# Kernel optimization log

Hardware: AMD Instinct MI355X
Metric: run time of the kernel (lower is better)

## Reference

```python
import jax, jax.numpy as jnp
import numpy as np
from jax import lax

T, B, V, E, HID, K = 512, 256, 50000, 300, 512, 9
H = HID // 2  # per-direction LSTM hidden size


def setup_inputs() -> dict:
    key = jax.random.key(0)
    ks = jax.random.split(key, 16)
    input_ids = jax.random.randint(ks[0], (T, B), 0, V, dtype=jnp.int32)
    lens = jax.random.randint(ks[1], (B,), T // 2, T + 1, dtype=jnp.int32)
    seq_lengths = jnp.sort(lens)[::-1].at[0].set(T)  # sorted desc, max == T
    label_ids = jax.random.randint(ks[2], (T, B), 0, K, dtype=jnp.int32)
    s = 0.1
    emb_table = jax.random.normal(ks[3], (V, E), jnp.float32) * s
    W_ih_f = jax.random.normal(ks[4], (4 * H, E), jnp.float32) * s
    W_hh_f = jax.random.normal(ks[5], (4 * H, H), jnp.float32) * s
    b_f = jax.random.normal(ks[6], (4 * H,), jnp.float32) * s  # b_ih + b_hh fused
    W_ih_b = jax.random.normal(ks[7], (4 * H, E), jnp.float32) * s
    W_hh_b = jax.random.normal(ks[8], (4 * H, H), jnp.float32) * s
    b_b = jax.random.normal(ks[9], (4 * H,), jnp.float32) * s
    W_out = jax.random.normal(ks[10], (K, HID), jnp.float32) * s
    b_out = jax.random.normal(ks[11], (K,), jnp.float32) * s
    start_trans = jax.random.normal(ks[12], (K,), jnp.float32) * s
    end_trans = jax.random.normal(ks[13], (K,), jnp.float32) * s
    trans = jax.random.normal(ks[14], (K, K), jnp.float32) * s
    return dict(input_ids=input_ids, seq_lengths=seq_lengths, label_ids=label_ids,
                emb_table=emb_table, W_ih_f=W_ih_f, W_hh_f=W_hh_f, b_f=b_f,
                W_ih_b=W_ih_b, W_hh_b=W_hh_b, b_b=b_b, W_out=W_out, b_out=b_out,
                start_trans=start_trans, end_trans=end_trans, trans=trans)


def _run_lstm(x, maskf, W_ih, W_hh, b, reverse):
    # x: [T,B,E], maskf: [T,B] float. Precompute input projections (one big GEMM).
    xg = jnp.einsum('tbe,ge->tbg', x, W_ih) + b  # [T,B,4H]

    def step(carry, inp):
        h, c = carry
        xg_t, m = inp
        gates = xg_t + h @ W_hh.T
        i, f, g, o = jnp.split(gates, 4, axis=-1)
        c_new = jax.nn.sigmoid(f) * c + jax.nn.sigmoid(i) * jnp.tanh(g)
        h_new = jax.nn.sigmoid(o) * jnp.tanh(c_new)
        m = m[:, None]
        return (m * h_new + (1 - m) * h, m * c_new + (1 - m) * c), m * h_new + (1 - m) * h

    init = (jnp.zeros((B, H), x.dtype), jnp.zeros((B, H), x.dtype))
    _, hs = lax.scan(step, init, (xg, maskf), reverse=reverse)
    return hs  # [T,B,H]


def reference(input_ids, seq_lengths, label_ids, emb_table, W_ih_f, W_hh_f, b_f,
              W_ih_b, W_hh_b, b_b, W_out, b_out, start_trans, end_trans, trans):
    maskf = (jnp.arange(T)[:, None] < seq_lengths[None, :]).astype(emb_table.dtype)  # [T,B]
    maskb = maskf.astype(bool)

    embeds = emb_table[input_ids]  # [T,B,E]
    h_f = _run_lstm(embeds, maskf, W_ih_f, W_hh_f, b_f, reverse=False)
    h_b = _run_lstm(embeds, maskf, W_ih_b, W_hh_b, b_b, reverse=True)
    lstm_out = jnp.concatenate([h_f, h_b], axis=-1)  # [T,B,HID]
    emissions = jnp.einsum('tbh,kh->tbk', lstm_out, W_out) + b_out  # [T,B,K]

    b_idx = jnp.arange(B)
    # --- CRF numerator (gold path score) ---
    num = start_trans[label_ids[0]] + emissions[0, b_idx, label_ids[0]]
    trans_sc = trans[label_ids[:-1], label_ids[1:]]  # [T-1,B]
    emit_sc = jnp.take_along_axis(emissions[1:], label_ids[1:, :, None], axis=2)[..., 0]
    num = num + jnp.sum((trans_sc + emit_sc) * maskf[1:], axis=0)
    last_tags = label_ids[seq_lengths - 1, b_idx]
    num = num + end_trans[last_tags]

    # --- CRF denominator (forward algorithm, log-sum-exp scan) ---
    def fwd_step(alpha, inp):
        em_t, m = inp
        nxt = jax.nn.logsumexp(alpha[:, :, None] + trans[None], axis=1) + em_t
        return jnp.where(m[:, None].astype(bool), nxt, alpha), None

    alpha0 = start_trans[None] + emissions[0]  # [B,K]
    alpha, _ = lax.scan(fwd_step, alpha0, (emissions[1:], maskf[1:]))
    denom = jax.nn.logsumexp(alpha + end_trans[None], axis=1)
    loss = -jnp.sum(num - denom)  # torchcrf reduction='sum', model negates llh

    # --- Viterbi decode ---
    def vit_step(score, inp):
        em_t, m = inp
        brd = score[:, :, None] + trans[None]  # [B,K_prev,K_next]
        idx = jnp.argmax(brd, axis=1)          # [B,K]
        nxt = jnp.max(brd, axis=1) + em_t
        return jnp.where(m[:, None].astype(bool), nxt, score), idx

    score0 = start_trans[None] + emissions[0]
    score, hist = lax.scan(vit_step, score0, (emissions[1:], maskf[1:]))  # hist [T-1,B,K]
    best_last = jnp.argmax(score + end_trans[None], axis=1)  # [B] tag at last valid pos

    def back_step(tag, inp):
        h_t, m_next = inp
        new = jnp.where(m_next.astype(bool),
                        jnp.take_along_axis(h_t, tag[:, None], axis=1)[:, 0],
                        best_last)
        return new, new

    _, preds = lax.scan(back_step, best_last, (hist, maskf[1:]), reverse=True)  # [T-1,B]
    pred_ids = jnp.concatenate([preds, best_last[None]], axis=0)  # [T,B]
    pred_ids = jnp.where(maskb, pred_ids, 0)
    return loss, pred_ids
```

## Files before the change

### kernel.cpp

```cpp
#include <hip/hip_runtime.h>
#include <math.h>

#define TT 512
#define BB 256
#define EE 300
#define KK 9
#define HH 256
#define GG 1024
#define CHS 64
#define NCH (TT/CHS)

#define OFF_XG ((size_t)0)
#define OFF_WT (OFF_XG + (size_t)2*CHS*BB*GG)
#define OFF_HS (OFF_WT + (size_t)2*64*1024*4)
#define OFF_CS (OFF_HS + (size_t)2*BB*HH)
#define OFF_EF (OFF_CS + (size_t)2*BB*HH)
#define OFF_EB (OFF_EF + (size_t)BB*TT*KK)
#define OFF_ND (OFF_EB + (size_t)BB*TT*KK)

#define DOT4(a_,b_) ((a_).x*(b_).x + (a_).y*(b_).y + (a_).z*(b_).z + (a_).w*(b_).w)
#define FMA4(acc_, w_, h_) do { \
    acc_ = fmaf((w_).x, (h_).x, acc_); \
    acc_ = fmaf((w_).y, (h_).y, acc_); \
    acc_ = fmaf((w_).z, (h_).z, acc_); \
    acc_ = fmaf((w_).w, (h_).w, acc_); } while (0)

__global__ __launch_bounds__(1024) void wtrans_kernel(
    const float* __restrict__ Wf, const float* __restrict__ Wb, float* __restrict__ Wt)
{
  int idx = blockIdx.x * 1024 + threadIdx.x;
  int dir = idx >> 16;
  int r   = (idx >> 6) & 1023;
  int k4  = idx & 63;
  const float* W = dir ? Wb : Wf;
  float4 v = *(const float4*)&W[(size_t)r * HH + k4 * 4];
  ((float4*)Wt)[(size_t)dir * 65536 + (size_t)k4 * 1024 + r] = v;
}

__global__ __launch_bounds__(256) void gemm_xg_kernel(
    const int* __restrict__ ids, const float* __restrict__ emb,
    const float* __restrict__ W_ih_f, const float* __restrict__ W_ih_b,
    const float* __restrict__ b_f, const float* __restrict__ b_b,
    float* __restrict__ xgc, int ci)
{
  __shared__ float As[60][132];
  __shared__ float Ws[60][132];
  __shared__ int tokid[128];
  const int tid = threadIdx.x;
  const int bx  = blockIdx.x;
  const int dir = bx >> 8;
  const int rem = bx & 255;
  const int rt  = rem & 127;
  const int nth = rem >> 7;
  const float* W_ih = dir ? W_ih_b : W_ih_f;
  const float* bias = dir ? b_b : b_f;

  if (tid < 128) {
    int m = rt * 128 + tid;
    int sidx = ci * CHS + (m >> 8);
    int t = dir ? (TT - 1 - sidx) : sidx;
    tokid[tid] = ids[t * BB + (m & 255)];
  }
  __syncthreads();

  const int ty = tid >> 4, tx = tid & 15;
  for (int nt = nth * 4; nt < nth * 4 + 4; ++nt) {
    float acc[8][8];
    #pragma unroll
    for (int a_ = 0; a_ < 8; ++a_)
      #pragma unroll
      for (int b_ = 0; b_ < 8; ++b_) acc[a_][b_] = 0.f;

    for (int kc = 0; kc < 5; ++kc) {
      __syncthreads();
      for (int i = tid; i < 128 * 15; i += 256) {
        int mm = i / 15, kq = i - mm * 15;
        float4 v = *(const float4*)&emb[(size_t)tokid[mm] * EE + kc * 60 + kq * 4];
        As[kq*4+0][mm] = v.x; As[kq*4+1][mm] = v.y;
        As[kq*4+2][mm] = v.z; As[kq*4+3][mm] = v.w;
      }
      for (int i = tid; i < 128 * 15; i += 256) {
        int nn = i / 15, kq = i - nn * 15;
        float4 v = *(const float4*)&W_ih[(size_t)(nt*128+nn) * EE + kc * 60 + kq * 4];
        Ws[kq*4+0][nn] = v.x; Ws[kq*4+1][nn] = v.y;
        Ws[kq*4+2][nn] = v.z; Ws[kq*4+3][nn] = v.w;
      }
      __syncthreads();
      for (int kk = 0; kk < 60; ++kk) {
        float4 a0 = *(const float4*)&As[kk][ty*8];
        float4 a1 = *(const float4*)&As[kk][ty*8+4];
        float4 w0 = *(const float4*)&Ws[kk][tx*8];
        float4 w1 = *(const float4*)&Ws[kk][tx*8+4];
        float av[8]  = {a0.x,a0.y,a0.z,a0.w,a1.x,a1.y,a1.z,a1.w};
        float wv8[8] = {w0.x,w0.y,w0.z,w0.w,w1.x,w1.y,w1.z,w1.w};
        #pragma unroll
        for (int im = 0; im < 8; ++im)
          #pragma unroll
          for (int in = 0; in < 8; ++in) acc[im][in] += av[im] * wv8[in];
      }
    }
    #pragma unroll
    for (int im = 0; im < 8; ++im) {
      int m = ty*8 + im;
      int n = nt*128 + tx*8;
      float4 o0, o1;
      o0.x = acc[im][0] + bias[n+0]; o0.y = acc[im][1] + bias[n+1];
      o0.z = acc[im][2] + bias[n+2]; o0.w = acc[im][3] + bias[n+3];
      o1.x = acc[im][4] + bias[n+4]; o1.y = acc[im][5] + bias[n+5];
      o1.z = acc[im][6] + bias[n+6]; o1.w = acc[im][7] + bias[n+7];
      float* dst = &xgc[(size_t)(dir*16384 + rt*128 + m) * GG + n];
      *(float4*)dst = o0; *(float4*)(dst+4) = o1;
    }
  }
}

__global__ __launch_bounds__(1024, 1) void rec_chunk_kernel(
    const float* __restrict__ xgc, const float* __restrict__ Wt,
    const int* __restrict__ lens,
    float* __restrict__ hst, float* __restrict__ cst,
    float* __restrict__ emisf, float* __restrict__ emisb,
    const float* __restrict__ W_out, const float* __restrict__ b_out, int ci)
{
  __shared__ __align__(16) float hring[2][2][272];
  __shared__ __align__(16) float Wo[KK][256];

  const int tid  = threadIdx.x;
  const int bid  = blockIdx.x;
  const int dir  = (bid & 7) >> 2;
  const int grp  = (bid >> 3) * 4 + (bid & 3);
  const int b0   = grp * 2;
  const int lane = tid & 63;
  const int wv   = tid >> 6;
  const int rg   = wv * 16 + (lane & 15);
  const int kseg = (lane >> 4) & 3;
  const bool cellLane = (lane & 48) == 0;
  float* emis = dir ? emisb : emisf;

  for (int i = tid; i < KK * 64; i += 1024) {
    int k = i >> 6, q = i & 63;
    *(float4*)&Wo[k][q*4] = *(const float4*)&W_out[(size_t)k * 512 + dir*256 + q*4];
  }

  int eb = 0, ek = 0, es = 0;
  const bool edo = tid < 2 * KK * 16;
  if (edo) { int q = tid; eb = q / 144; q -= eb * 144; ek = q >> 4; es = q & 15; }
  const float ebias = (edo && dir == 0) ? b_out[ek] : 0.f;

  int len2[2];
  #pragma unroll
  for (int b = 0; b < 2; ++b) len2[b] = lens[b0 + b];

  float creg[2] = {0.f,0.f}, hreg[2] = {0.f,0.f};
  if (cellLane) {
    if (ci > 0) {
      #pragma unroll
      for (int b = 0; b < 2; ++b) {
        hreg[b] = hst[((size_t)dir*BB + b0 + b) * HH + rg];
        creg[b] = cst[((size_t)dir*BB + b0 + b) * HH + rg];
      }
    }
    #pragma unroll
    for (int b = 0; b < 2; ++b)
      hring[0][b][rg + ((rg >> 6) << 2)] = hreg[b];
  }
  __syncthreads();

  const float4* wp = (const float4*)Wt + (size_t)dir * 65536
                   + (size_t)(kseg * 16) * 1024 + rg;

  for (int sl = 0; sl < CHS; ++sl) {
    const int s = ci * CHS + sl;
    const int t = dir ? (TT - 1 - s) : s;
    const int cur = sl & 1, nxt = cur ^ 1;

    float xv[4][2];
    if (cellLane) {
      const float* xb = xgc + ((size_t)dir*(CHS*BB) + (size_t)sl*BB + b0) * GG + rg;
      #pragma unroll
      for (int q = 0; q < 4; ++q)
        #pragma unroll
        for (int b = 0; b < 2; ++b)
          xv[q][b] = __builtin_nontemporal_load(&xb[(size_t)b * GG + q * 256]);
    }

    float acc[4][2];
    #pragma unroll
    for (int q = 0; q < 4; ++q) { acc[q][0] = 0.f; acc[q][1] = 0.f; }

    const float4* hb = (const float4*)&hring[0][0][0] + cur * (2*68) + kseg * 17;
    float4 w0 = wp[0], w1 = wp[256], w2 = wp[512], w3 = wp[768];
    #pragma unroll 5
    for (int i = 0; i < 15; ++i) {
      const float4* wn = wp + (size_t)(i + 1) * 1024;
      float4 n0 = wn[0], n1 = wn[256], n2 = wn[512], n3 = wn[768];
      float4 h0 = hb[i], h1 = hb[68 + i];
      FMA4(acc[0][0], w0, h0); FMA4(acc[0][1], w0, h1);
      FMA4(acc[1][0], w1, h0); FMA4(acc[1][1], w1, h1);
      FMA4(acc[2][0], w2, h0); FMA4(acc[2][1], w2, h1);
      FMA4(acc[3][0], w3, h0); FMA4(acc[3][1], w3, h1);
      w0 = n0; w1 = n1; w2 = n2; w3 = n3;
    }
    {
      float4 h0 = hb[15], h1 = hb[68 + 15];
      FMA4(acc[0][0], w0, h0); FMA4(acc[0][1], w0, h1);
      FMA4(acc[1][0], w1, h0); FMA4(acc[1][1], w1, h1);
      FMA4(acc[2][0], w2, h0); FMA4(acc[2][1], w2, h1);
      FMA4(acc[3][0], w3, h0); FMA4(acc[3][1], w3, h1);
    }

    #pragma unroll
    for (int q = 0; q < 4; ++q)
      #pragma unroll
      for (int b = 0; b < 2; ++b) {
        float v = acc[q][b];
        v += __shfl_xor(v, 16);
        v += __shfl_xor(v, 32);
        acc[q][b] = v;
      }

    if (cellLane) {
      #pragma unroll
      for (int b = 0; b < 2; ++b) {
        float gi = acc[0][b] + xv[0][b];
        float gf = acc[1][b] + xv[1][b];
        float gg = acc[2][b] + xv[2][b];
        float go = acc[3][b] + xv[3][b];
        float si = 1.f / (1.f + expf(-gi));
        float sf = 1.f / (1.f + expf(-gf));
        float so = 1.f / (1.f + expf(-go));
        float cn = sf * creg[b] + si * tanhf(gg);
        float hn = so * tanhf(cn);
        bool m = t < len2[b];
        hreg[b] = m ? hn : hreg[b];
        creg[b] = m ? cn : creg[b];
        hring[nxt][b][rg + ((rg >> 6) << 2)] = hreg[b];
      }
    }
    __syncthreads();

    if (edo) {
      float r = 0.f;
      #pragma unroll
      for (int i4 = 0; i4 < 4; ++i4) {
        float4 h4 = *(const float4*)&hring[nxt][eb][es*4 + i4*68];
        float4 w4 = *(const float4*)&Wo[ek][es*4 + i4*64];
        r += DOT4(h4, w4);
      }
      r += __shfl_xor(r, 8); r += __shfl_xor(r, 4);
      r += __shfl_xor(r, 2); r += __shfl_xor(r, 1);
      if (es == 0)
        __builtin_nontemporal_store(r + ebias,
            &emis[((size_t)(b0 + eb) * TT + t) * KK + ek]);
    }
  }

  if (cellLane) {
    #pragma unroll
    for (int b = 0; b < 2; ++b) {
      hst[((size_t)dir*BB + b0 + b) * HH + rg] = hreg[b];
      cst[((size_t)dir*BB + b0 + b) * HH + rg] = creg[b];
    }
  }
}

__global__ __launch_bounds__(64) void crf_kernel(
    const float* __restrict__ emis_f, const float* __restrict__ emis_b2,
    const int* __restrict__ labels, const int* __restrict__ lens,
    const float* __restrict__ start_trans, const float* __restrict__ end_trans,
    const float* __restrict__ trans,
    float* __restrict__ numden, float* __restrict__ outp)
{
  const int b = blockIdx.x;
  const int lane = threadIdx.x;
  __shared__ __align__(16) float em[TT * KK];
  __shared__ unsigned char hist[TT * KK];
  const float4* ef = (const float4*)(emis_f + (size_t)b * TT * KK);
  const float4* eb = (const float4*)(emis_b2 + (size_t)b * TT * KK);
  for (int i = lane; i < TT*KK/4; i += 64) {
    float4 a = ef[i], c = eb[i];
    float4 o; o.x = a.x+c.x; o.y = a.y+c.y; o.z = a.z+c.z; o.w = a.w+c.w;
    ((float4*)em)[i] = o;
  }
  const int len = lens[b];
  const int k = lane < KK ? lane : KK-1;
  float tc[KK];
  #pragma unroll
  for (int jj = 0; jj < KK; ++jj) tc[jj] = trans[jj*KK + k];
  __syncthreads();

  float nacc = 0.f;
  for (int t = lane; t < TT; t += 64) {
    int lt = labels[t*BB + b];
    if (t == 0) nacc += start_trans[lt] + em[lt];
    else if (t < len) nacc += trans[labels[(t-1)*BB + b]*KK + lt] + em[t*KK + lt];
  }
  if (lane == 0) nacc += end_trans[labels[(size_t)(len-1)*BB + b]];
  #pragma unroll
  for (int off = 32; off; off >>= 1) nacc += __shfl_down(nacc, off);

  float alpha[KK], score[KK];
  #pragma unroll
  for (int jj = 0; jj < KK; ++jj) {
    float v = start_trans[jj] + em[jj];
    alpha[jj] = v; score[jj] = v;
  }
  for (int t = 1; t < TT; ++t) {
    float av[KK]; float mx = -1e30f;
    #pragma unroll
    for (int jj = 0; jj < KK; ++jj) { av[jj] = alpha[jj] + tc[jj]; mx = fmaxf(mx, av[jj]); }
    float ssum = 0.f;
    #pragma unroll
    for (int jj = 0; jj < KK; ++jj) ssum += expf(av[jj] - mx);
    float e_tk = em[t*KK + k];
    float na = mx + logf(ssum) + e_tk;
    float best = -1e30f; int bj = 0;
    #pragma unroll
    for (int jj = 0; jj < KK; ++jj) {
      float sv = score[jj] + tc[jj];
      if (sv > best) { best = sv; bj = jj; }
    }
    float ns = best + e_tk;
    bool msk = t < len;
    na = msk ? na : alpha[k];
    ns = msk ? ns : score[k];
    if (lane < KK) hist[(t-1)*KK + lane] = (unsigned char)bj;
    #pragma unroll
    for (int jj = 0; jj < KK; ++jj) { alpha[jj] = __shfl(na, jj); score[jj] = __shfl(ns, jj); }
  }
  float dm = -1e30f;
  #pragma unroll
  for (int jj = 0; jj < KK; ++jj) dm = fmaxf(dm, alpha[jj] + end_trans[jj]);
  float dsum = 0.f;
  #pragma unroll
  for (int jj = 0; jj < KK; ++jj) dsum += expf(alpha[jj] + end_trans[jj] - dm);
  float denom = dm + logf(dsum);
  int bl_ = 0; float bs = -1e30f;
  #pragma unroll
  for (int jj = 0; jj < KK; ++jj) {
    float v = score[jj] + end_trans[jj];
    if (v > bs) { bs = v; bl_ = jj; }
  }
  if (lane == 0) numden[b] = nacc - denom;
  __syncthreads();
  if (lane == 0) {
    int tag = bl_;
    outp[1 + (size_t)(TT-1)*BB + b] = ((TT-1) < len) ? (float)bl_ : 0.f;
    for (int s = TT-2; s >= 0; --s) {
      tag = ((s+1) < len) ? (int)hist[s*KK + tag] : bl_;
      outp[1 + (size_t)s*BB + b] = (s < len) ? (float)tag : 0.f;
    }
  }
}

__global__ __launch_bounds__(256) void loss_reduce_kernel(
    const float* __restrict__ numden, float* __restrict__ out)
{
  __shared__ float sh[256];
  int tid = threadIdx.x;
  sh[tid] = numden[tid];
  __syncthreads();
  for (int s = 128; s > 0; s >>= 1) {
    if (tid < s) sh[tid] += sh[tid + s];
    __syncthreads();
  }
  if (tid == 0) out[0] = -sh[0];
}

extern "C" void kernel_launch(void* const* d_in, const int* in_sizes, int n_in,
                              void* d_out, int out_size, void* d_ws, size_t ws_size,
                              hipStream_t stream)
{
  const int*   ids    = (const int*)d_in[0];
  const int*   lens   = (const int*)d_in[1];
  const int*   labels = (const int*)d_in[2];
  const float* emb    = (const float*)d_in[3];
  const float* W_ih_f = (const float*)d_in[4];
  const float* W_hh_f = (const float*)d_in[5];
  const float* b_f    = (const float*)d_in[6];
  const float* W_ih_b = (const float*)d_in[7];
  const float* W_hh_b = (const float*)d_in[8];
  const float* b_b    = (const float*)d_in[9];
  const float* W_out  = (const float*)d_in[10];
  const float* b_out  = (const float*)d_in[11];
  const float* s_tr   = (const float*)d_in[12];
  const float* e_tr   = (const float*)d_in[13];
  const float* trans  = (const float*)d_in[14];
  float* out = (float*)d_out;

  float* ws = (float*)d_ws;
  float* xgc    = ws + OFF_XG;
  float* Wt     = ws + OFF_WT;
  float* hst    = ws + OFF_HS;
  float* cst    = ws + OFF_CS;
  float* emis_f = ws + OFF_EF;
  float* emis_b = ws + OFF_EB;
  float* numden = ws + OFF_ND;

  wtrans_kernel<<<128, 1024, 0, stream>>>(W_hh_f, W_hh_b, Wt);

  for (int ci = 0; ci < NCH; ++ci) {
    gemm_xg_kernel<<<512, 256, 0, stream>>>(ids, emb, W_ih_f, W_ih_b, b_f, b_b, xgc, ci);
    rec_chunk_kernel<<<256, 1024, 0, stream>>>(xgc, Wt, lens, hst, cst,
                                               emis_f, emis_b, W_out, b_out, ci);
  }

  crf_kernel<<<BB, 64, 0, stream>>>(emis_f, emis_b, labels, lens, s_tr, e_tr, trans, numden, out);
  loss_reduce_kernel<<<1, 256, 0, stream>>>(numden, out);
}
```

Before: 7.220 ms.

## Keep part of recurrent weights resident in registers and LDS across timesteps

The recurrent step streams the W_hh slice from global memory every timestep. This keeps the first 3 of 16 k-blocks in registers (48 floats per thread) and the next 2 in a 128KB LDS buffer loaded once per launch. The remaining blocks still stream from global with software prefetch. This is meant to cut per-step global/L2 traffic on the serial critical path. It costs much higher register pressure, a large LDS allocation, and a longer kernel prologue.

```diff
diff --git a/kernel.cpp b/kernel.cpp
--- a/kernel.cpp
+++ b/kernel.cpp
@@ -123,6 +123,7 @@
 {
   __shared__ __align__(16) float hring[2][2][272];
   __shared__ __align__(16) float Wo[KK][256];
+  __shared__ __align__(16) float4 WL[2 * 4 * 1024];
 
   const int tid  = threadIdx.x;
   const int bid  = blockIdx.x;
@@ -141,6 +142,16 @@
     *(float4*)&Wo[k][q*4] = *(const float4*)&W_out[(size_t)k * 512 + dir*256 + q*4];
   }
 
+  {
+    const float4* wtd = (const float4*)Wt + (size_t)dir * 65536;
+    for (int i = tid; i < 8192; i += 1024) {
+      int j  = i >> 12;
+      int ks = (i >> 10) & 3;
+      int row = i & 1023;
+      WL[i] = wtd[(size_t)(ks * 16 + 3 + j) * 1024 + row];
+    }
+  }
+
   int eb = 0, ek = 0, es = 0;
   const bool edo = tid < 2 * KK * 16;
   if (edo) { int q = tid; eb = q / 144; q -= eb * 144; ek = q >> 4; es = q & 15; }
@@ -163,10 +174,20 @@
     for (int b = 0; b < 2; ++b)
       hring[0][b][rg + ((rg >> 6) << 2)] = hreg[b];
   }
-  __syncthreads();
 
   const float4* wp = (const float4*)Wt + (size_t)dir * 65536
                    + (size_t)(kseg * 16) * 1024 + rg;
+
+  float4 wres[12];
+  #pragma unroll
+  for (int i = 0; i < 3; ++i)
+    #pragma unroll
+    for (int q = 0; q < 4; ++q)
+      wres[i*4 + q] = wp[(size_t)i * 1024 + q * 256];
+
+  __syncthreads();
+
+  const int wlbase = kseg * 1024 + rg;
 
   for (int sl = 0; sl < CHS; ++sl) {
     const int s = ci * CHS + sl;
@@ -188,9 +209,32 @@
     for (int q = 0; q < 4; ++q) { acc[q][0] = 0.f; acc[q][1] = 0.f; }
 
     const float4* hb = (const float4*)&hring[0][0][0] + cur * (2*68) + kseg * 17;
-    float4 w0 = wp[0], w1 = wp[256], w2 = wp[512], w3 = wp[768];
-    #pragma unroll 5
-    for (int i = 0; i < 15; ++i) {
+
+    float4 w0 = wp[(size_t)5*1024 +   0];
+    float4 w1 = wp[(size_t)5*1024 + 256];
+    float4 w2 = wp[(size_t)5*1024 + 512];
+    float4 w3 = wp[(size_t)5*1024 + 768];
+
+    #pragma unroll
+    for (int i = 0; i < 3; ++i) {
+      float4 h0 = hb[i], h1 = hb[68 + i];
+      FMA4(acc[0][0], wres[i*4+0], h0); FMA4(acc[0][1], wres[i*4+0], h1);
+      FMA4(acc[1][0], wres[i*4+1], h0); FMA4(acc[1][1], wres[i*4+1], h1);
+      FMA4(acc[2][0], wres[i*4+2], h0); FMA4(acc[2][1], wres[i*4+2], h1);
+      FMA4(acc[3][0], wres[i*4+3], h0); FMA4(acc[3][1], wres[i*4+3], h1);
+    }
+    #pragma unroll
+    for (int i = 3; i < 5; ++i) {
+      const float4* wl = &WL[(i - 3) * 4096 + wlbase];
+      float4 v0 = wl[0], v1 = wl[256], v2 = wl[512], v3 = wl[768];
+      float4 h0 = hb[i], h1 = hb[68 + i];
+      FMA4(acc[0][0], v0, h0); FMA4(acc[0][1], v0, h1);
+      FMA4(acc[1][0], v1, h0); FMA4(acc[1][1], v1, h1);
+      FMA4(acc[2][0], v2, h0); FMA4(acc[2][1], v2, h1);
+      FMA4(acc[3][0], v3, h0); FMA4(acc[3][1], v3, h1);
+    }
+    #pragma unroll
+    for (int i = 5; i < 15; ++i) {
       const float4* wn = wp + (size_t)(i + 1) * 1024;
       float4 n0 = wn[0], n1 = wn[256], n2 = wn[512], n3 = wn[768];
       float4 h0 = hb[i], h1 = hb[68 + i];
```

After: 15.42 ms. +113.6%, slower.
